# Kernel optimization log

Measured on AMD Instinct MI355X. Metric: run time of the kernel, lower is better.

The kernel has to match this reference:

```python
import jax, jax.numpy as jnp
import numpy as np

C, H, W = 8, 8, 8
A = 6            # action_dim
LATENT = 64
HID = 64
GRU_IN = HID + A + LATENT  # 134


def _conv(x, w):
    return jax.lax.conv_general_dilated(
        x, w, (1, 1), 'VALID', dimension_numbers=('NCHW', 'OIHW', 'NCHW'))


def setup_inputs() -> dict:
    key = jax.random.key(0)
    ks = jax.random.split(key, 20)
    B, N, T = 64, 10, 128
    s_h = jax.random.normal(ks[0], (B, N, T, C, H, W), jnp.float32)
    a_h = jax.random.randint(ks[1], (B, N, T), 0, A).astype(jnp.int64)
    b_z = jax.random.normal(ks[2], (B, LATENT), jnp.float32)
    s = 0.05
    p = {
        'conv1_w': jax.random.normal(ks[3], (32, C, 3, 3)) * s,
        'conv1_b': jnp.zeros((32,)),
        'conv2_w': jax.random.normal(ks[4], (32, 32, 3, 3)) * s,
        'conv2_b': jnp.zeros((32,)),
        'fc_w': jax.random.normal(ks[5], (HID, 32 * 4 * 4)) * s,
        'fc_b': jnp.zeros((HID,)),
        'emb': jax.random.normal(ks[6], (A, A)) * s,
        'gru_wih': jax.random.normal(ks[7], (3 * HID, GRU_IN)) * s,
        'gru_whh': jax.random.normal(ks[8], (3 * HID, HID)) * s,
        'gru_bih': jnp.zeros((3 * HID,)),
        'gru_bhh': jnp.zeros((3 * HID,)),
        'mlp1_w': jax.random.normal(ks[9], (HID, HID)) * s,
        'mlp1_b': jnp.zeros((HID,)),
        'mlp2_w': jax.random.normal(ks[10], (A, HID)) * s,
        'mlp2_b': jnp.zeros((A,)),
    }
    return {'s_h': s_h, 'a_h': a_h, 'b_z': b_z, **p}


def reference(s_h, a_h, b_z, conv1_w, conv1_b, conv2_w, conv2_b, fc_w, fc_b,
              emb, gru_wih, gru_whh, gru_bih, gru_bhh,
              mlp1_w, mlp1_b, mlp2_w, mlp2_b):
    B, N = s_h.shape[0], s_h.shape[1]
    T = a_h.shape[2]
    BN = B * N

    # action mask, [B, N, T, 1]
    action_masks = (a_h != A - 1)[..., None].astype(jnp.float32)

    # --- state encoder on first frame only ---
    s0 = s_h[:, :, 0].reshape(BN, C, H, W)
    x = jax.nn.relu(_conv(s0, conv1_w) + conv1_b[:, None, None])
    x = jax.nn.relu(_conv(x, conv2_w) + conv2_b[:, None, None])
    x = x.reshape(BN, -1)                       # [BN, 512]
    state_emb = jax.nn.relu(x @ fc_w.T + fc_b)  # [BN, HID]

    bz = jnp.broadcast_to(b_z[:, None, :], (B, N, LATENT)).reshape(BN, LATENT)

    h0 = jnp.zeros((BN, HID), s_h.dtype)
    act0 = jnp.full((BN,), A - 1, jnp.int32)

    def step(carry, _):
        h, act = carry
        a_emb = emb[act]                                          # [BN, A]
        inp = jnp.concatenate([state_emb, a_emb, bz], axis=-1)    # [BN, GRU_IN]
        gx = inp @ gru_wih.T + gru_bih
        gh = h @ gru_whh.T + gru_bhh
        xr, xz, xn = jnp.split(gx, 3, axis=-1)
        hr, hz, hn = jnp.split(gh, 3, axis=-1)
        r = jax.nn.sigmoid(xr + hr)
        z = jax.nn.sigmoid(xz + hz)
        n = jnp.tanh(xn + r * hn)
        h_new = (1.0 - z) * n + z * h
        hid = jnp.tanh(h_new @ mlp1_w.T + mlp1_b)
        logits = hid @ mlp2_w.T + mlp2_b                          # [BN, A]
        next_act = jax.lax.stop_gradient(jnp.argmax(logits, axis=-1)).astype(jnp.int32)
        return (h_new, next_act), logits

    (_, _), logits_seq = jax.lax.scan(step, (h0, act0), None, length=T - 1)
    # logits_seq: [T-1, BN, A] -> [B, N, T-1, A]
    logits_all = jnp.transpose(logits_seq, (1, 0, 2)).reshape(B, N, T - 1, A)
    return logits_all, action_masks
```

## Files before the change

kernel.cpp:

```cpp
#include <hip/hip_runtime.h>

#define A_DIM 6
#define HID_D 64
#define LATENT_D 64
#define GRU_IN_D 134
#define T_STEPS 128
#define N_ENV 10
#define BN_TOT 640

typedef float f2 __attribute__((ext_vector_type(2)));

__device__ __forceinline__ float fast_sigmoid(float x) {
    return __builtin_amdgcn_rcpf(1.0f + __builtin_amdgcn_exp2f(-1.4426950408889634f * x));
}
__device__ __forceinline__ float fast_tanh(float x) {
    return 1.0f - 2.0f * __builtin_amdgcn_rcpf(1.0f + __builtin_amdgcn_exp2f(2.8853900817779268f * x));
}

template<int CTRL>
__device__ __forceinline__ float dppadd(float v) {
    int t = __builtin_amdgcn_update_dpp(0, __builtin_bit_cast(int, v), CTRL, 0xf, 0xf, true);
    return v + __builtin_bit_cast(float, t);
}
__device__ __forceinline__ float wave_reduce_add(float v) {
    v = dppadd<0x111>(v);
    v = dppadd<0x112>(v);
    v = dppadd<0x114>(v);
    v = dppadd<0x118>(v);
    v = dppadd<0x142>(v);
    v = dppadd<0x143>(v);
    return __builtin_bit_cast(float, __builtin_amdgcn_readlane(__builtin_bit_cast(int, v), 63));
}

__global__ __launch_bounds__(128, 1)
void policy_kernel(const float* __restrict__ s_h,
                   const int*   __restrict__ a_h,
                   const float* __restrict__ b_z,
                   const float* __restrict__ conv1_w, const float* __restrict__ conv1_b,
                   const float* __restrict__ conv2_w, const float* __restrict__ conv2_b,
                   const float* __restrict__ fc_w,    const float* __restrict__ fc_b,
                   const float* __restrict__ emb,
                   const float* __restrict__ gru_wih, const float* __restrict__ gru_whh,
                   const float* __restrict__ gru_bih, const float* __restrict__ gru_bhh,
                   const float* __restrict__ mlp1_w,  const float* __restrict__ mlp1_b,
                   const float* __restrict__ mlp2_w,  const float* __restrict__ mlp2_b,
                   float* __restrict__ logits_out, float* __restrict__ mask_out)
{
    __shared__ __align__(16) float s0[512];
    __shared__ __align__(16) float a1[1152];
    __shared__ __align__(16) float a2[512];
    __shared__ __align__(16) float pfc[128];
    __shared__ __align__(16) float semb[64];
    __shared__ __align__(16) float gxc[192];
    __shared__ __align__(16) float atab[6*192];
    __shared__ __align__(16) float hpriv[2][64];
    __shared__ __align__(16) float4 pex[2][2][64];

    const int bn  = blockIdx.x;
    const int tid = threadIdx.x;
    const int j   = tid & 63;
    const int w   = tid >> 6;

    mask_out[bn * T_STEPS + tid] = (a_h[bn * T_STEPS + tid] != (A_DIM - 1)) ? 1.0f : 0.0f;

    {
        const float* src = s_h + (size_t)bn * T_STEPS * 512;
        #pragma unroll
        for (int i = 0; i < 4; ++i) s0[tid + i * 128] = src[tid + i * 128];
    }
    __syncthreads();

    for (int i = tid; i < 1152; i += 128) {
        const int oc = i / 36, r = i % 36, oh = r / 6, ow = r % 6;
        float sum = conv1_b[oc];
        const float* wp = conv1_w + oc * 72;
        #pragma unroll
        for (int ic = 0; ic < 8; ++ic)
            #pragma unroll
            for (int kh = 0; kh < 3; ++kh)
                #pragma unroll
                for (int kw = 0; kw < 3; ++kw)
                    sum = fmaf(s0[ic * 64 + (oh + kh) * 8 + (ow + kw)],
                               wp[ic * 9 + kh * 3 + kw], sum);
        a1[i] = fmaxf(sum, 0.0f);
    }
    __syncthreads();

    for (int i = tid; i < 512; i += 128) {
        const int oc = i / 16, r = i % 16, oh = r / 4, ow = r % 4;
        float sum = conv2_b[oc];
        const float* wp = conv2_w + oc * 288;
        for (int ic = 0; ic < 32; ++ic)
            #pragma unroll
            for (int kh = 0; kh < 3; ++kh)
                #pragma unroll
                for (int kw = 0; kw < 3; ++kw)
                    sum = fmaf(a1[ic * 36 + (oh + kh) * 6 + (ow + kw)],
                               wp[ic * 9 + kh * 3 + kw], sum);
        a2[i] = fmaxf(sum, 0.0f);
    }
    __syncthreads();

    {
        const float* wp = fc_w + j * 512 + w * 256;
        const float* ap = a2 + w * 256;
        float s0a = 0.f, s1a = 0.f, s2a = 0.f, s3a = 0.f;
        for (int k = 0; k < 256; k += 4) {
            s0a = fmaf(ap[k + 0], wp[k + 0], s0a);
            s1a = fmaf(ap[k + 1], wp[k + 1], s1a);
            s2a = fmaf(ap[k + 2], wp[k + 2], s2a);
            s3a = fmaf(ap[k + 3], wp[k + 3], s3a);
        }
        pfc[tid] = (s0a + s1a) + (s2a + s3a);
    }
    __syncthreads();
    if (tid < 64) semb[tid] = fmaxf(pfc[tid] + pfc[tid + 64] + fc_b[tid], 0.0f);
    __syncthreads();

    {
        const float* bz = b_z + (size_t)(bn / N_ENV) * LATENT_D;
        for (int g = tid; g < 192; g += 128) {
            float sum = gru_bih[g] + ((g < 128) ? gru_bhh[g] : 0.0f);
            const float* wp = gru_wih + g * GRU_IN_D;
            for (int k = 0; k < 64; ++k) sum = fmaf(semb[k], wp[k], sum);
            for (int k = 0; k < 64; ++k) sum = fmaf(bz[k], wp[70 + k], sum);
            gxc[g] = sum;
        }
    }
    for (int i = tid; i < 6 * 192; i += 128) {
        const int a = i / 192, g = i % 192;
        float sum = 0.0f;
        #pragma unroll
        for (int q = 0; q < 6; ++q)
            sum = fmaf(emb[a * 6 + q], gru_wih[g * GRU_IN_D + 64 + q], sum);
        atab[i] = sum;
    }
    __syncthreads();

    f2 wr[16], wz[16], wn[16], w1[16];
    {
        const float* pr = gru_whh + (size_t)j * 64 + 32 * w;
        const float* pz = gru_whh + (size_t)(64 + j) * 64 + 32 * w;
        const float* pn = gru_whh + (size_t)(128 + j) * 64 + 32 * w;
        const float* p1 = mlp1_w + (size_t)j * 64 + 32 * w;
        #pragma unroll
        for (int i = 0; i < 8; ++i) {
            float4 v;
            v = ((const float4*)pr)[i]; wr[2*i] = (f2){v.x, v.y}; wr[2*i+1] = (f2){v.z, v.w};
            v = ((const float4*)pz)[i]; wz[2*i] = (f2){v.x, v.y}; wz[2*i+1] = (f2){v.z, v.w};
            v = ((const float4*)pn)[i]; wn[2*i] = (f2){v.x, v.y}; wn[2*i+1] = (f2){v.z, v.w};
            v = ((const float4*)p1)[i]; w1[2*i] = (f2){v.x, v.y}; w1[2*i+1] = (f2){v.z, v.w};
        }
    }
    const float gxr = gxc[j], gxz = gxc[64 + j], gxn = gxc[128 + j];
    const float bhn = gru_bhh[128 + j];
    const float b1j = mlp1_b[j];
    float ar[6], az[6], an[6], m2c[6], b2[6];
    #pragma unroll
    for (int a = 0; a < 6; ++a) {
        ar[a] = atab[a * 192 + j];
        az[a] = atab[a * 192 + 64 + j];
        an[a] = atab[a * 192 + 128 + j];
        m2c[a] = mlp2_w[a * 64 + j];
        b2[a] = mlp2_b[a];
    }

    float hprev = 0.0f;
    float hr_c = 0.0f, hz_c = 0.0f, hn_c = bhn;
    int act = A_DIM - 1;
    float* lout = logits_out + (size_t)bn * (T_STEPS - 1) * A_DIM;
    const float4* hp4 = (const float4*)(&hpriv[w][0]) + w * 8;

    for (int t = 0; t < T_STEPS - 1; ++t) {
        float sr = ar[0], sz = az[0], sn = an[0];
        #pragma unroll
        for (int a = 1; a < 6; ++a) {
            const bool c = (act == a);
            sr = c ? ar[a] : sr; sz = c ? az[a] : sz; sn = c ? an[a] : sn;
        }
        const float r = fast_sigmoid(gxr + sr + hr_c);
        const float z = fast_sigmoid(gxz + sz + hz_c);
        const float n = fast_tanh(fmaf(r, hn_c, gxn + sn));
        const float hnew = fmaf(z, hprev - n, n);
        hprev = hnew;

        __builtin_amdgcn_wave_barrier();
        hpriv[w][j] = hnew;
        __builtin_amdgcn_wave_barrier();

        f2 pr = {0.f, 0.f}, pz = {0.f, 0.f}, pn = {0.f, 0.f}, p1 = {0.f, 0.f};
        #pragma unroll
        for (int i = 0; i < 8; ++i) {
            const float4 hv = hp4[i];
            const f2 ha = (f2){hv.x, hv.y};
            const f2 hb = (f2){hv.z, hv.w};
            pr += ha * wr[2*i]; pr += hb * wr[2*i+1];
            pz += ha * wz[2*i]; pz += hb * wz[2*i+1];
            pn += ha * wn[2*i]; pn += hb * wn[2*i+1];
            p1 += ha * w1[2*i]; p1 += hb * w1[2*i+1];
        }
        const float mr = pr.x + pr.y, mz = pz.x + pz.y;
        const float mn = pn.x + pn.y, m1 = p1.x + p1.y;

        pex[t & 1][w][j] = (float4){mr, mz, mn, m1};
        __syncthreads();
        const float4 o = pex[t & 1][w ^ 1][j];
        hr_c = mr + o.x;
        hz_c = mz + o.y;
        hn_c = mn + o.z + bhn;
        const float hid = fast_tanh(m1 + o.w + b1j);

        const float l0 = wave_reduce_add(hid * m2c[0]) + b2[0];
        const float l1 = wave_reduce_add(hid * m2c[1]) + b2[1];
        const float l2 = wave_reduce_add(hid * m2c[2]) + b2[2];
        const float l3 = wave_reduce_add(hid * m2c[3]) + b2[3];
        const float l4 = wave_reduce_add(hid * m2c[4]) + b2[4];
        const float l5 = wave_reduce_add(hid * m2c[5]) + b2[5];

        float best = l0; int bi = 0;
        if (l1 > best) { best = l1; bi = 1; }
        if (l2 > best) { best = l2; bi = 2; }
        if (l3 > best) { best = l3; bi = 3; }
        if (l4 > best) { best = l4; bi = 4; }
        if (l5 > best) { best = l5; bi = 5; }
        act = bi;

        if (tid < A_DIM) {
            const float outv = (j == 0) ? l0 : (j == 1) ? l1 : (j == 2) ? l2
                             : (j == 3) ? l3 : (j == 4) ? l4 : l5;
            lout[t * A_DIM + j] = outv;
        }
    }
}

extern "C" void kernel_launch(void* const* d_in, const int* in_sizes, int n_in,
                              void* d_out, int out_size, void* d_ws, size_t ws_size,
                              hipStream_t stream) {
    const float* s_h     = (const float*)d_in[0];
    const int*   a_h     = (const int*)  d_in[1];
    const float* b_z     = (const float*)d_in[2];
    const float* conv1_w = (const float*)d_in[3];
    const float* conv1_b = (const float*)d_in[4];
    const float* conv2_w = (const float*)d_in[5];
    const float* conv2_b = (const float*)d_in[6];
    const float* fc_w    = (const float*)d_in[7];
    const float* fc_b    = (const float*)d_in[8];
    const float* emb     = (const float*)d_in[9];
    const float* gru_wih = (const float*)d_in[10];
    const float* gru_whh = (const float*)d_in[11];
    const float* gru_bih = (const float*)d_in[12];
    const float* gru_bhh = (const float*)d_in[13];
    const float* mlp1_w  = (const float*)d_in[14];
    const float* mlp1_b  = (const float*)d_in[15];
    const float* mlp2_w  = (const float*)d_in[16];
    const float* mlp2_b  = (const float*)d_in[17];

    float* out = (float*)d_out;
    float* logits_out = out;
    float* mask_out   = out + (size_t)BN_TOT * (T_STEPS - 1) * A_DIM;

    policy_kernel<<<BN_TOT, 128, 0, stream>>>(
        s_h, a_h, b_z, conv1_w, conv1_b, conv2_w, conv2_b, fc_w, fc_b, emb,
        gru_wih, gru_whh, gru_bih, gru_bhh, mlp1_w, mlp1_b, mlp2_w, mlp2_b,
        logits_out, mask_out);
}
```

Baseline: 517.0 us.

## Run GRU recurrence in a single wave to drop per-step block barrier

```diff
diff --git a/kernel.cpp b/kernel.cpp
--- a/kernel.cpp
+++ b/kernel.cpp
@@ -53,8 +53,7 @@
     __shared__ __align__(16) float semb[64];
     __shared__ __align__(16) float gxc[192];
     __shared__ __align__(16) float atab[6*192];
-    __shared__ __align__(16) float hpriv[2][64];
-    __shared__ __align__(16) float4 pex[2][2][64];
+    __shared__ __align__(16) float hbuf[64];
 
     const int bn  = blockIdx.x;
     const int tid = threadIdx.x;
@@ -137,14 +136,16 @@
     }
     __syncthreads();
 
-    f2 wr[16], wz[16], wn[16], w1[16];
-    {
-        const float* pr = gru_whh + (size_t)j * 64 + 32 * w;
-        const float* pz = gru_whh + (size_t)(64 + j) * 64 + 32 * w;
-        const float* pn = gru_whh + (size_t)(128 + j) * 64 + 32 * w;
-        const float* p1 = mlp1_w + (size_t)j * 64 + 32 * w;
-        #pragma unroll
-        for (int i = 0; i < 8; ++i) {
+    if (w == 1) return;
+
+    f2 wr[32], wz[32], wn[32], w1[32];
+    {
+        const float* pr = gru_whh + (size_t)j * 64;
+        const float* pz = gru_whh + (size_t)(64 + j) * 64;
+        const float* pn = gru_whh + (size_t)(128 + j) * 64;
+        const float* p1 = mlp1_w + (size_t)j * 64;
+        #pragma unroll
+        for (int i = 0; i < 16; ++i) {
             float4 v;
             v = ((const float4*)pr)[i]; wr[2*i] = (f2){v.x, v.y}; wr[2*i+1] = (f2){v.z, v.w};
             v = ((const float4*)pz)[i]; wz[2*i] = (f2){v.x, v.y}; wz[2*i+1] = (f2){v.z, v.w};
@@ -169,7 +170,7 @@
     float hr_c = 0.0f, hz_c = 0.0f, hn_c = bhn;
     int act = A_DIM - 1;
     float* lout = logits_out + (size_t)bn * (T_STEPS - 1) * A_DIM;
-    const float4* hp4 = (const float4*)(&hpriv[w][0]) + w * 8;
+    const float4* hb = (const float4*)hbuf;
 
     for (int t = 0; t < T_STEPS - 1; ++t) {
         float sr = ar[0], sz = az[0], sn = an[0];
@@ -185,30 +186,24 @@
         hprev = hnew;
 
         __builtin_amdgcn_wave_barrier();
-        hpriv[w][j] = hnew;
+        hbuf[j] = hnew;
         __builtin_amdgcn_wave_barrier();
 
-        f2 pr = {0.f, 0.f}, pz = {0.f, 0.f}, pn = {0.f, 0.f}, p1 = {0.f, 0.f};
-        #pragma unroll
-        for (int i = 0; i < 8; ++i) {
-            const float4 hv = hp4[i];
+        f2 p1 = {0.f, 0.f}, pr = {0.f, 0.f}, pz = {0.f, 0.f}, pn = {0.f, 0.f};
+        #pragma unroll
+        for (int i = 0; i < 16; ++i) {
+            const float4 hv = hb[i];
             const f2 ha = (f2){hv.x, hv.y};
-            const f2 hb = (f2){hv.z, hv.w};
-            pr += ha * wr[2*i]; pr += hb * wr[2*i+1];
-            pz += ha * wz[2*i]; pz += hb * wz[2*i+1];
-            pn += ha * wn[2*i]; pn += hb * wn[2*i+1];
-            p1 += ha * w1[2*i]; p1 += hb * w1[2*i+1];
-        }
-        const float mr = pr.x + pr.y, mz = pz.x + pz.y;
-        const float mn = pn.x + pn.y, m1 = p1.x + p1.y;
-
-        pex[t & 1][w][j] = (float4){mr, mz, mn, m1};
-        __syncthreads();
-        const float4 o = pex[t & 1][w ^ 1][j];
-        hr_c = mr + o.x;
-        hz_c = mz + o.y;
-        hn_c = mn + o.z + bhn;
-        const float hid = fast_tanh(m1 + o.w + b1j);
+            const f2 hc = (f2){hv.z, hv.w};
+            p1 += ha * w1[2*i]; p1 += hc * w1[2*i+1];
+            pr += ha * wr[2*i]; pr += hc * wr[2*i+1];
+            pz += ha * wz[2*i]; pz += hc * wz[2*i+1];
+            pn += ha * wn[2*i]; pn += hc * wn[2*i+1];
+        }
+        hr_c = pr.x + pr.y;
+        hz_c = pz.x + pz.y;
+        hn_c = pn.x + pn.y + bhn;
+        const float hid = fast_tanh(p1.x + p1.y + b1j);
 
         const float l0 = wave_reduce_add(hid * m2c[0]) + b2[0];
         const float l1 = wave_reduce_add(hid * m2c[1]) + b2[1];
@@ -225,7 +220,7 @@
         if (l5 > best) { best = l5; bi = 5; }
         act = bi;
 
-        if (tid < A_DIM) {
+        if (j < A_DIM) {
             const float outv = (j == 0) ? l0 : (j == 1) ? l1 : (j == 2) ? l2
                              : (j == 3) ? l3 : (j == 4) ? l4 : l5;
             lout[t * A_DIM + j] = outv;
```

Result: faster. 482.9 us (-6.6%).
